# Optimization experiments

Hardware: AMD Instinct MI355X
Metric: run time of the kernel (lower is better)

The kernel has to match this reference:

```python
import jax, jax.numpy as jnp
import numpy as np

B, S, E, N = 2, 2048, 768, 12
H = E // N

def setup_inputs() -> dict:
    key = jax.random.key(0)
    k1, k2, k3, k4, k5 = jax.random.split(key, 5)
    x = jax.random.normal(k1, (B, S, E), dtype=jnp.float32)
    Wqkv = jax.random.normal(k2, (E, 3 * E), dtype=jnp.float32) * (1.0 / np.sqrt(E))
    bqkv = jax.random.normal(k3, (3 * E,), dtype=jnp.float32) * 0.02
    Wproj = jax.random.normal(k4, (E, E), dtype=jnp.float32) * (1.0 / np.sqrt(E))
    bproj = jax.random.normal(k5, (E,), dtype=jnp.float32) * 0.02
    mask = jnp.tril(jnp.ones((S, S), dtype=jnp.int32))[None, None]  # (1,1,S,S) causal
    return {"mask": mask, "x": x, "Wqkv": Wqkv, "bqkv": bqkv, "Wproj": Wproj, "bproj": bproj}

def reference(mask, x, Wqkv, bqkv, Wproj, bproj):
    Bx, Sx, Ex = x.shape
    Hd = Ex // N
    qkv = x @ Wqkv + bqkv                       # (B,S,3E)
    q, k, v = jnp.split(qkv, 3, axis=-1)
    q = q.reshape(Bx, Sx, N, Hd).transpose(0, 2, 1, 3)  # (B,N,S,H)
    k = k.reshape(Bx, Sx, N, Hd).transpose(0, 2, 1, 3)
    v = v.reshape(Bx, Sx, N, Hd).transpose(0, 2, 1, 3)
    att = jnp.einsum('bnsh,bnth->bnst', q, k) / jnp.sqrt(jnp.float32(Hd))
    att = jnp.where(mask == 0, -jnp.inf, att)   # causal masked_fill
    p = jax.nn.softmax(att, axis=-1)            # dropout p=0.0 -> identity
    y = jnp.einsum('bnst,bnth->bnsh', p, v)     # (B,N,S,H)
    y = y.transpose(0, 2, 1, 3).reshape(Bx, Sx, Ex)
    return y @ Wproj + bproj
```

## Files before the change

kernel.cpp:

```cpp
#include <hip/hip_runtime.h>
#include <hip/hip_bf16.h>
#include <math.h>

#define S_LEN 2048
#define E_DIM 768
#define NHEAD 12
#define HDIM 64
#define BATCH 2
#define MROWS (BATCH * S_LEN)
#define KDIM E_DIM
#define NBN (BATCH * NHEAD)
#define NTASKS 768

typedef __attribute__((ext_vector_type(8))) short bf16x8;
typedef __attribute__((ext_vector_type(4))) float f32x4;

__device__ inline unsigned short f2bf(float f) {
    __hip_bfloat16 h = __float2bfloat16(f);
    union { __hip_bfloat16 b; unsigned short u; } v; v.b = h;
    return v.u;
}

__global__ __launch_bounds__(256) void prep(
    const float* __restrict__ x, unsigned short* __restrict__ Xb,
    const float* __restrict__ Wqkv, unsigned short* __restrict__ WqkvT,
    const float* __restrict__ Wproj, unsigned short* __restrict__ WprojT)
{
    __shared__ float t[32][33];
    const int blk = blockIdx.x, tid = threadIdx.x;
    if (blk < 3072) {
        const int i = blk * 256 + tid;
        const float4 a = ((const float4*)x)[i];
        ushort4 o;
        o.x = f2bf(a.x); o.y = f2bf(a.y); o.z = f2bf(a.z); o.w = f2bf(a.w);
        ((ushort4*)Xb)[i] = o;
        return;
    }
    const float* W; unsigned short* WT; int N, bt;
    if (blk < 3072 + 1728) { bt = blk - 3072; N = 3 * E_DIM; W = Wqkv; WT = WqkvT; }
    else                   { bt = blk - 4800; N = E_DIM;     W = Wproj; WT = WprojT; }
    const int bx = bt % (N / 32), by = bt / (N / 32);
    const int k0 = by * 32, n0 = bx * 32;
    const int r = tid >> 3, c4 = (tid & 7) * 4;
    const float4 v = *(const float4*)&W[(size_t)(k0 + r) * N + n0 + c4];
    t[r][c4 + 0] = v.x; t[r][c4 + 1] = v.y; t[r][c4 + 2] = v.z; t[r][c4 + 3] = v.w;
    __syncthreads();
    ushort4 o;
    o.x = f2bf(t[c4 + 0][r]); o.y = f2bf(t[c4 + 1][r]);
    o.z = f2bf(t[c4 + 2][r]); o.w = f2bf(t[c4 + 3][r]);
    *(ushort4*)&WT[(size_t)(n0 + r) * KDIM + k0 + c4] = o;
}

template <int EPI, int BM, int BN>
__global__ __launch_bounds__(256, 3) void gemm_t(
    const unsigned short* __restrict__ A, const unsigned short* __restrict__ BT,
    const float* __restrict__ bias, void* __restrict__ out0,
    void* __restrict__ out1, void* __restrict__ out2, int Nn)
{
    constexpr int MF = BM / 32;
    constexpr int NF = BN / 32;
    __shared__ unsigned short As[BM * 64];
    __shared__ unsigned short Bs[BN * 64];
    const int tid = threadIdx.x;
    const int lane = tid & 63;
    const int wid = tid >> 6;
    const int lr = lane & 15, lg = lane >> 4;
    const int wr = wid >> 1, wc = wid & 1;
    const int m0 = blockIdx.y * BM;
    const int n0 = blockIdx.x * BN;
    const int srow = lane >> 3, scol = (lane & 7) * 8;

    f32x4 acc[MF][NF];
    #pragma unroll
    for (int i = 0; i < MF; ++i)
        #pragma unroll
        for (int j = 0; j < NF; ++j) acc[i][j] = (f32x4){0.f, 0.f, 0.f, 0.f};

    for (int k0 = 0; k0 < KDIM; k0 += 64) {
        __syncthreads();
        #pragma unroll
        for (int c = 0; c < MF; ++c) {
            const int chunk = wid * MF + c;
            const int row = chunk * 8 + srow;
            const unsigned short* ga = A + (size_t)(m0 + row) * KDIM + k0 + scol;
            __builtin_amdgcn_global_load_lds(
                (const __attribute__((address_space(1))) void*)ga,
                (__attribute__((address_space(3))) void*)&As[chunk * 512], 16, 0, 0);
        }
        #pragma unroll
        for (int c = 0; c < NF; ++c) {
            const int chunk = wid * NF + c;
            const int row = chunk * 8 + srow;
            const unsigned short* gb = BT + (size_t)(n0 + row) * KDIM + k0 + scol;
            __builtin_amdgcn_global_load_lds(
                (const __attribute__((address_space(1))) void*)gb,
                (__attribute__((address_space(3))) void*)&Bs[chunk * 512], 16, 0, 0);
        }
        __syncthreads();

        #pragma unroll
        for (int kk = 0; kk < 2; ++kk) {
            bf16x8 af[MF], bf[NF];
            #pragma unroll
            for (int mt = 0; mt < MF; ++mt)
                af[mt] = *(const bf16x8*)&As[(wr * (BM / 2) + mt * 16 + lr) * 64 + kk * 32 + lg * 8];
            #pragma unroll
            for (int nt = 0; nt < NF; ++nt)
                bf[nt] = *(const bf16x8*)&Bs[(wc * (BN / 2) + nt * 16 + lr) * 64 + kk * 32 + lg * 8];
            #pragma unroll
            for (int mt = 0; mt < MF; ++mt)
                #pragma unroll
                for (int nt = 0; nt < NF; ++nt)
                    acc[mt][nt] = __builtin_amdgcn_mfma_f32_16x16x32_bf16(
                        af[mt], bf[nt], acc[mt][nt], 0, 0, 0);
        }
    }

    #pragma unroll
    for (int mt = 0; mt < MF; ++mt) {
        const int rowbase = m0 + wr * (BM / 2) + mt * 16 + lg * 4;
        #pragma unroll
        for (int nt = 0; nt < NF; ++nt) {
            const int col = n0 + wc * (BN / 2) + nt * 16 + lr;
            if (EPI == 0) {
                float* O = (float*)out0;
                const float bv = bias[col];
                #pragma unroll
                for (int r = 0; r < 4; ++r)
                    O[(size_t)(rowbase + r) * Nn + col] = acc[mt][nt][r] + bv;
            } else {
                const int which = col / E_DIM;
                const int rem = col % E_DIM;
                const int head = rem >> 6, h = rem & 63;
                const float bv = bias[col];
                if (which == 2) {
                    const int b = rowbase >> 11, s0 = rowbase & (S_LEN - 1);
                    const int scolv = (s0 & ~63) | ((s0 & 63) ^ ((h & 7) << 3));
                    unsigned short* VT = (unsigned short*)out2;
                    ushort4 pk;
                    pk.x = f2bf(acc[mt][nt][0] + bv);
                    pk.y = f2bf(acc[mt][nt][1] + bv);
                    pk.z = f2bf(acc[mt][nt][2] + bv);
                    pk.w = f2bf(acc[mt][nt][3] + bv);
                    *(ushort4*)&VT[((size_t)(b * NHEAD + head) * HDIM + h) * S_LEN + scolv] = pk;
                } else {
                    unsigned short* dst = (which == 0) ? (unsigned short*)out0
                                                       : (unsigned short*)out1;
                    const float sc = (which == 0) ? 0.125f : 1.0f;
                    #pragma unroll
                    for (int r = 0; r < 4; ++r) {
                        const int m = rowbase + r;
                        const int b = m >> 11, s = m & (S_LEN - 1);
                        const int hh = (which == 1) ? (h ^ ((s & 7) << 3)) : h;
                        dst[(((size_t)(b * NHEAD + head) * S_LEN) + s) * HDIM + hh] =
                            f2bf((acc[mt][nt][r] + bv) * sc);
                    }
                }
            }
        }
    }
}

__global__ __launch_bounds__(256, 4) void attn_mfma(
    const unsigned short* __restrict__ Qb, const unsigned short* __restrict__ Kb,
    const unsigned short* __restrict__ VTb, unsigned short* __restrict__ Y,
    float* __restrict__ ws_o, float* __restrict__ ws_l)
{
    __shared__ unsigned short smem[5 * 4096];

    const int tid = threadIdx.x;
    const int lane = tid & 63;
    const int wid = tid >> 6;
    const int lr = lane & 15;
    const int lg = lane >> 4;

    unsigned short* const Pw = smem + 16384 + wid * 1024;

    const int task = blockIdx.x;
    const int bn = task % NBN;
    const int rest = task / NBN;
    const int jj = rest & 15, half = rest >> 4;
    const int b = bn / NHEAD, n = bn % NHEAD;

    const unsigned short* Kg = Kb + (size_t)bn * S_LEN * HDIM;
    const unsigned short* Vg = VTb + (size_t)bn * HDIM * S_LEN;

    auto run_pass = [&](int qb, int t0, int t1, int mode) {
        const size_t qoff = ((size_t)bn * S_LEN + (qb * 64 + wid * 16 + lr)) * HDIM;
        const bf16x8 qB0 = *(const bf16x8*)(Qb + qoff + lg * 8);
        const bf16x8 qB1 = *(const bf16x8*)(Qb + qoff + 32 + lg * 8);

        f32x4 o[4];
        #pragma unroll
        for (int ht = 0; ht < 4; ++ht) o[ht] = (f32x4){0.f, 0.f, 0.f, 0.f};
        float lacc = 0.f;

        __syncthreads();
        #pragma unroll
        for (int e = 0; e < 2; ++e) {
            const int chunk = wid * 2 + e;
            __builtin_amdgcn_global_load_lds(
                (const __attribute__((address_space(1))) void*)
                    (Kg + (size_t)t0 * 4096 + chunk * 512 + lane * 8),
                (__attribute__((address_space(3))) void*)&smem[chunk * 512], 16, 0, 0);
            __builtin_amdgcn_global_load_lds(
                (const __attribute__((address_space(1))) void*)
                    (Vg + (size_t)(chunk * 8 + (lane >> 3)) * S_LEN + t0 * 64 + (lane & 7) * 8),
                (__attribute__((address_space(3))) void*)&smem[8192 + chunk * 512], 16, 0, 0);
        }

        int cur = 0;
        for (int t = t0; t < t1; ++t) {
            __syncthreads();
            if (t + 1 < t1) {
                #pragma unroll
                for (int e = 0; e < 2; ++e) {
                    const int chunk = wid * 2 + e;
                    __builtin_amdgcn_global_load_lds(
                        (const __attribute__((address_space(1))) void*)
                            (Kg + (size_t)(t + 1) * 4096 + chunk * 512 + lane * 8),
                        (__attribute__((address_space(3))) void*)
                            &smem[(cur ^ 1) * 4096 + chunk * 512], 16, 0, 0);
                    __builtin_amdgcn_global_load_lds(
                        (const __attribute__((address_space(1))) void*)
                            (Vg + (size_t)(chunk * 8 + (lane >> 3)) * S_LEN + (t + 1) * 64
                                + (lane & 7) * 8),
                        (__attribute__((address_space(3))) void*)
                            &smem[8192 + (cur ^ 1) * 4096 + chunk * 512], 16, 0, 0);
                }
            }

            const unsigned short* Kc = smem + cur * 4096;
            const unsigned short* Vc = smem + 8192 + cur * 4096;

            f32x4 s[4];
            __builtin_amdgcn_s_setprio(1);
            #pragma unroll
            for (int ct = 0; ct < 4; ++ct) {
                const int kr = ct * 16 + lr;
                const int xo = (kr & 7) << 3;
                const bf16x8 kb0 = *(const bf16x8*)&Kc[kr * 64 + ((lg * 8) ^ xo)];
                const bf16x8 kb1 = *(const bf16x8*)&Kc[kr * 64 + ((32 + lg * 8) ^ xo)];
                f32x4 a = (f32x4){0.f, 0.f, 0.f, 0.f};
                a = __builtin_amdgcn_mfma_f32_16x16x32_bf16(kb0, qB0, a, 0, 0, 0);
                a = __builtin_amdgcn_mfma_f32_16x16x32_bf16(kb1, qB1, a, 0, 0, 0);
                s[ct] = a;
            }
            __builtin_amdgcn_s_setprio(0);

            if (t == qb) {
                const int q = qb * 64 + wid * 16 + lr;
                #pragma unroll
                for (int ct = 0; ct < 4; ++ct) {
                    #pragma unroll
                    for (int r = 0; r < 4; ++r) {
                        const int k = t * 64 + ct * 16 + lg * 4 + r;
                        if (k > q) s[ct][r] = -1e30f;
                    }
                }
            }

            const int pxo = (lr & 7) << 3;
            #pragma unroll
            for (int ct = 0; ct < 4; ++ct) {
                const float p0 = __expf(s[ct][0] - 8.f);
                const float p1 = __expf(s[ct][1] - 8.f);
                const float p2 = __expf(s[ct][2] - 8.f);
                const float p3 = __expf(s[ct][3] - 8.f);
                lacc += (p0 + p1) + (p2 + p3);
                ushort4 pk;
                pk.x = f2bf(p0); pk.y = f2bf(p1); pk.z = f2bf(p2); pk.w = f2bf(p3);
                *(ushort4*)&Pw[lr * 64 + ((ct * 16 + lg * 4) ^ pxo)] = pk;
            }

            const bf16x8 pa0 = *(const bf16x8*)&Pw[lr * 64 + ((lg * 8) ^ pxo)];
            const bf16x8 pa1 = *(const bf16x8*)&Pw[lr * 64 + ((32 + lg * 8) ^ pxo)];
            __builtin_amdgcn_s_setprio(1);
            #pragma unroll
            for (int ht = 0; ht < 4; ++ht) {
                const int h = ht * 16 + lr;
                const int xo = (h & 7) << 3;
                const bf16x8 vb0 = *(const bf16x8*)&Vc[h * 64 + ((lg * 8) ^ xo)];
                const bf16x8 vb1 = *(const bf16x8*)&Vc[h * 64 + ((32 + lg * 8) ^ xo)];
                o[ht] = __builtin_amdgcn_mfma_f32_16x16x32_bf16(pa0, vb0, o[ht], 0, 0, 0);
                o[ht] = __builtin_amdgcn_mfma_f32_16x16x32_bf16(pa1, vb1, o[ht], 0, 0, 0);
            }
            __builtin_amdgcn_s_setprio(0);
            cur ^= 1;
        }

        lacc += __shfl_xor(lacc, 16, 64);
        lacc += __shfl_xor(lacc, 32, 64);

        if (mode == 2) {
            float invl[4];
            #pragma unroll
            for (int r = 0; r < 4; ++r)
                invl[r] = 1.f / __shfl(lacc, lg * 4 + r, 64);
            #pragma unroll
            for (int r = 0; r < 4; ++r) {
                const int qrow = qb * 64 + wid * 16 + lg * 4 + r;
                unsigned short* yrow =
                    Y + ((size_t)(b * S_LEN + qrow)) * E_DIM + n * HDIM;
                #pragma unroll
                for (int ht = 0; ht < 4; ++ht)
                    yrow[ht * 16 + lr] = f2bf(o[ht][r] * invl[r]);
            }
        } else {
            const size_t m = (size_t)(bn * 16 + (qb - 16)) * 2 + mode;
            float* wo = ws_o + m * 4096;
            const int rowl = wid * 16 + lg * 4;
            #pragma unroll
            for (int ht = 0; ht < 4; ++ht)
                #pragma unroll
                for (int r = 0; r < 4; ++r)
                    wo[(rowl + r) * 64 + ht * 16 + lr] = o[ht][r];
            if (lg == 0) ws_l[m * 64 + wid * 16 + lr] = lacc;
        }
    };

    if (half == 0) {
        run_pass(31 - jj, 0, 16, 0);
    } else {
        run_pass(31 - jj, 16, 32 - jj, 1);
        run_pass(jj, 0, jj + 1, 2);
    }
}

__global__ __launch_bounds__(256) void attn_merge(
    const float* __restrict__ ws_o, const float* __restrict__ ws_l,
    unsigned short* __restrict__ Y)
{
    const int m = blockIdx.x;
    const int bn = m / 16, qb = 16 + (m % 16);
    const int b = bn / NHEAD, n = bn % NHEAD;
    const int tid = threadIdx.x;
    const int r = tid >> 2, h0 = (tid & 3) * 16;

    const float* o0 = ws_o + ((size_t)m * 2 + 0) * 4096 + r * 64 + h0;
    const float* o1 = ws_o + ((size_t)m * 2 + 1) * 4096 + r * 64 + h0;
    const float l = ws_l[((size_t)m * 2 + 0) * 64 + r] +
                    ws_l[((size_t)m * 2 + 1) * 64 + r];
    const float inv = 1.f / l;
    unsigned short* yrow =
        Y + ((size_t)(b * S_LEN + qb * 64 + r)) * E_DIM + n * HDIM + h0;
    #pragma unroll
    for (int q = 0; q < 16; q += 4) {
        const float4 a = *(const float4*)(o0 + q);
        const float4 c = *(const float4*)(o1 + q);
        ushort4 pk;
        pk.x = f2bf((a.x + c.x) * inv); pk.y = f2bf((a.y + c.y) * inv);
        pk.z = f2bf((a.z + c.z) * inv); pk.w = f2bf((a.w + c.w) * inv);
        *(ushort4*)&yrow[q] = pk;
    }
}

extern "C" void kernel_launch(void* const* d_in, const int* in_sizes, int n_in,
                              void* d_out, int out_size, void* d_ws, size_t ws_size,
                              hipStream_t stream) {
    const float* x     = (const float*)d_in[1];
    const float* Wqkv  = (const float*)d_in[2];
    const float* bqkv  = (const float*)d_in[3];
    const float* Wproj = (const float*)d_in[4];
    const float* bproj = (const float*)d_in[5];
    float* out = (float*)d_out;

    const size_t per = (size_t)BATCH * NHEAD * S_LEN * HDIM;
    unsigned short* Xb     = (unsigned short*)d_ws;
    unsigned short* WqkvT  = Xb + (size_t)MROWS * E_DIM;
    unsigned short* WprojT = WqkvT + (size_t)3 * E_DIM * E_DIM;
    unsigned short* Qb     = WprojT + (size_t)E_DIM * E_DIM;
    unsigned short* Kb     = Qb + per;
    unsigned short* VTb    = Kb + per;
    unsigned short* Yb     = VTb + per;
    float*          ws_o   = (float*)(Yb + (size_t)MROWS * E_DIM);
    float*          ws_l   = ws_o + (size_t)384 * 2 * 4096;

    prep<<<5376, 256, 0, stream>>>(x, Xb, Wqkv, WqkvT, Wproj, WprojT);
    gemm_t<1, 128, 96><<<dim3(3 * E_DIM / 96, MROWS / 128), 256, 0, stream>>>(
        Xb, WqkvT, bqkv, Qb, Kb, VTb, 3 * E_DIM);
    attn_mfma<<<NTASKS, 256, 0, stream>>>(Qb, Kb, VTb, Yb, ws_o, ws_l);
    attn_merge<<<384, 256, 0, stream>>>(ws_o, ws_l, Yb);
    gemm_t<0, 64, 64><<<dim3(E_DIM / 64, MROWS / 64), 256, 0, stream>>>(
        Yb, WprojT, bproj, out, nullptr, nullptr, E_DIM);
}
```

Baseline: 79.89 us.

## Fuse split-KV merge into attention via atomic arrival flags and remap blocks to XCDs

Removes the separate attn_merge kernel. Each of the two partial-pass blocks writes its partial O and row sums, then increments a per-tile atomic counter, and whichever block arrives second does the merge and normalisation and writes Y directly. The counters are zeroed by the first block of the QKV GEMM. The block-to-task mapping is also changed so that all tasks for one head land on the same XCD (blockIdx mod 8), which is meant to improve L2 reuse of K/V. The cost is extra fences, block syncs and atomics, and correctness depends on the flags being reset before every attention launch.

```diff
diff --git a/kernel.cpp b/kernel.cpp
--- a/kernel.cpp
+++ b/kernel.cpp
@@ -55,8 +55,12 @@
 __global__ __launch_bounds__(256, 3) void gemm_t(
     const unsigned short* __restrict__ A, const unsigned short* __restrict__ BT,
     const float* __restrict__ bias, void* __restrict__ out0,
-    void* __restrict__ out1, void* __restrict__ out2, int Nn)
+    void* __restrict__ out1, void* __restrict__ out2, int Nn,
+    unsigned int* __restrict__ flags)
 {
+    if (EPI == 1 && blockIdx.x == 0 && blockIdx.y == 0) {
+        for (int i = threadIdx.x; i < 384; i += 256) flags[i] = 0u;
+    }
     constexpr int MF = BM / 32;
     constexpr int NF = BN / 32;
     __shared__ unsigned short As[BM * 64];
@@ -164,7 +168,8 @@
 __global__ __launch_bounds__(256, 4) void attn_mfma(
     const unsigned short* __restrict__ Qb, const unsigned short* __restrict__ Kb,
     const unsigned short* __restrict__ VTb, unsigned short* __restrict__ Y,
-    float* __restrict__ ws_o, float* __restrict__ ws_l)
+    float* __restrict__ ws_o, float* __restrict__ ws_l,
+    unsigned int* __restrict__ flags)
 {
     __shared__ unsigned short smem[5 * 4096];
 
@@ -176,9 +181,10 @@
 
     unsigned short* const Pw = smem + 16384 + wid * 1024;
 
-    const int task = blockIdx.x;
-    const int bn = task % NBN;
-    const int rest = task / NBN;
+    const int B = blockIdx.x;
+    const int xcd = B & 7, slot = B >> 3;
+    const int bn = xcd + (slot >> 5) * 8;
+    const int rest = slot & 31;
     const int jj = rest & 15, half = rest >> 4;
     const int b = bn / NHEAD, n = bn % NHEAD;
 
@@ -307,15 +313,49 @@
                     yrow[ht * 16 + lr] = f2bf(o[ht][r] * invl[r]);
             }
         } else {
-            const size_t m = (size_t)(bn * 16 + (qb - 16)) * 2 + mode;
-            float* wo = ws_o + m * 4096;
+            const size_t m = (size_t)(bn * 16 + (qb - 16));
+            float* wo = ws_o + (m * 2 + mode) * 4096;
             const int rowl = wid * 16 + lg * 4;
             #pragma unroll
             for (int ht = 0; ht < 4; ++ht)
                 #pragma unroll
                 for (int r = 0; r < 4; ++r)
                     wo[(rowl + r) * 64 + ht * 16 + lr] = o[ht][r];
-            if (lg == 0) ws_l[m * 64 + wid * 16 + lr] = lacc;
+            if (lg == 0) ws_l[m * 128 + mode * 64 + wid * 16 + lr] = lacc;
+
+            __threadfence();
+            __syncthreads();
+            if (tid == 0) {
+                const unsigned old = atomicAdd(&flags[m], 1u);
+                *(unsigned*)smem = old;
+            }
+            __syncthreads();
+            const unsigned old = *(const unsigned*)smem;
+            if (old == 1) {
+                __threadfence();
+                const float* wo2 = ws_o + (m * 2 + (1 - mode)) * 4096;
+                #pragma unroll
+                for (int ht = 0; ht < 4; ++ht)
+                    #pragma unroll
+                    for (int r = 0; r < 4; ++r)
+                        o[ht][r] += wo2[(rowl + r) * 64 + ht * 16 + lr];
+                const float lother =
+                    ws_l[m * 128 + (1 - mode) * 64 + wid * 16 + lr];
+                const float ltot = lacc + lother;
+                float invl[4];
+                #pragma unroll
+                for (int r = 0; r < 4; ++r)
+                    invl[r] = 1.f / __shfl(ltot, lg * 4 + r, 64);
+                #pragma unroll
+                for (int r = 0; r < 4; ++r) {
+                    const int qrow = qb * 64 + wid * 16 + lg * 4 + r;
+                    unsigned short* yrow =
+                        Y + ((size_t)(b * S_LEN + qrow)) * E_DIM + n * HDIM;
+                    #pragma unroll
+                    for (int ht = 0; ht < 4; ++ht)
+                        yrow[ht * 16 + lr] = f2bf(o[ht][r] * invl[r]);
+                }
+            }
         }
     };
 
@@ -324,34 +364,6 @@
     } else {
         run_pass(31 - jj, 16, 32 - jj, 1);
         run_pass(jj, 0, jj + 1, 2);
-    }
-}
-
-__global__ __launch_bounds__(256) void attn_merge(
-    const float* __restrict__ ws_o, const float* __restrict__ ws_l,
-    unsigned short* __restrict__ Y)
-{
-    const int m = blockIdx.x;
-    const int bn = m / 16, qb = 16 + (m % 16);
-    const int b = bn / NHEAD, n = bn % NHEAD;
-    const int tid = threadIdx.x;
-    const int r = tid >> 2, h0 = (tid & 3) * 16;
-
-    const float* o0 = ws_o + ((size_t)m * 2 + 0) * 4096 + r * 64 + h0;
-    const float* o1 = ws_o + ((size_t)m * 2 + 1) * 4096 + r * 64 + h0;
-    const float l = ws_l[((size_t)m * 2 + 0) * 64 + r] +
-                    ws_l[((size_t)m * 2 + 1) * 64 + r];
-    const float inv = 1.f / l;
-    unsigned short* yrow =
-        Y + ((size_t)(b * S_LEN + qb * 64 + r)) * E_DIM + n * HDIM + h0;
-    #pragma unroll
-    for (int q = 0; q < 16; q += 4) {
-        const float4 a = *(const float4*)(o0 + q);
-        const float4 c = *(const float4*)(o1 + q);
-        ushort4 pk;
-        pk.x = f2bf((a.x + c.x) * inv); pk.y = f2bf((a.y + c.y) * inv);
-        pk.z = f2bf((a.z + c.z) * inv); pk.w = f2bf((a.w + c.w) * inv);
-        *(ushort4*)&yrow[q] = pk;
     }
 }
 
@@ -375,12 +387,12 @@
     unsigned short* Yb     = VTb + per;
     float*          ws_o   = (float*)(Yb + (size_t)MROWS * E_DIM);
     float*          ws_l   = ws_o + (size_t)384 * 2 * 4096;
+    unsigned int*   flags  = (unsigned int*)(ws_l + (size_t)384 * 128);
 
     prep<<<5376, 256, 0, stream>>>(x, Xb, Wqkv, WqkvT, Wproj, WprojT);
     gemm_t<1, 128, 96><<<dim3(3 * E_DIM / 96, MROWS / 128), 256, 0, stream>>>(
-        Xb, WqkvT, bqkv, Qb, Kb, VTb, 3 * E_DIM);
-    attn_mfma<<<NTASKS, 256, 0, stream>>>(Qb, Kb, VTb, Yb, ws_o, ws_l);
-    attn_merge<<<384, 256, 0, stream>>>(ws_o, ws_l, Yb);
+        Xb, WqkvT, bqkv, Qb, Kb, VTb, 3 * E_DIM, flags);
+    attn_mfma<<<NTASKS, 256, 0, stream>>>(Qb, Kb, VTb, Yb, ws_o, ws_l, flags);
     gemm_t<0, 64, 64><<<dim3(E_DIM / 64, MROWS / 64), 256, 0, stream>>>(
-        Yb, WprojT, bproj, out, nullptr, nullptr, E_DIM);
-}
+        Yb, WprojT, bproj, out, nullptr, nullptr, E_DIM, nullptr);
+}
```

After: 217.8 us. 173% more time.
